# Kernel tuning notes

Measured on AMD Instinct MI355X. Metric: run time of the kernel, lower is better.

Reference implementation:

```python
import jax, jax.numpy as jnp
import numpy as np

B, T, E, H = 2, 2048, 1024, 16
D = E // H  # head dim = 64


def setup_inputs() -> dict:
    key = jax.random.key(0)
    kx, kq, kk, kv, kw = jax.random.split(key, 5)
    # kaiming-normal-like init for per-head projections, xavier-like for output proj
    qkv_std = (2.0 / E) ** 0.5
    w_std = (6.0 / (E + E)) ** 0.5 / (3.0 ** 0.5)
    x = jax.random.normal(kx, (B, T, E), dtype=jnp.float32)
    Wq = jax.random.normal(kq, (H, E, D), dtype=jnp.float32) * qkv_std
    Wk = jax.random.normal(kk, (H, E, D), dtype=jnp.float32) * qkv_std
    Wv = jax.random.normal(kv, (H, E, D), dtype=jnp.float32) * qkv_std
    Wo = jax.random.normal(kw, (E, E), dtype=jnp.float32) * w_std
    return {"x": x, "Wq": Wq, "Wk": Wk, "Wv": Wv, "Wo": Wo}


def reference(x, Wq, Wk, Wv, Wo):
    # per-head projections, batched over heads: bte,hed->bhtd
    q = jnp.einsum('bte,hed->bhtd', x, Wq)
    k = jnp.einsum('bte,hed->bhtd', x, Wk)
    v = jnp.einsum('bte,hed->bhtd', x, Wv)
    scale = 1.0 / jnp.sqrt(jnp.asarray(D, dtype=q.dtype))
    scores = jnp.einsum('bhtd,bhTd->bhtT', q, k) * scale  # [B,H,T,T]
    attn = jax.nn.softmax(scores, axis=-1)
    heads = jnp.einsum('bhtT,bhTd->bhtd', attn, v)  # [B,H,T,D]
    # concat heads along feature dim (head order preserved)
    combined = heads.transpose(0, 2, 1, 3).reshape(B, T, E)
    return combined @ Wo + x
```

## Files before the change

### kernel.cpp

```cpp
#include <hip/hip_runtime.h>
#include <hip/hip_bf16.h>


#define B_ 2
#define T_ 2048
#define E_ 1024
#define H_ 16
#define D_ 64
#define VTS_ 2176
#define LD_ 72

typedef _Float16 h8 __attribute__((ext_vector_type(8)));
typedef float f32x4 __attribute__((ext_vector_type(4)));

union U4 { uint4 u; h8 h; };

__device__ __forceinline__ float h2f(unsigned short s) {
  _Float16 h;
  __builtin_memcpy(&h, &s, 2);
  return (float)h;
}

__device__ __forceinline__ unsigned short f2h(float f) {
  _Float16 h = (_Float16)f;
  unsigned short s;
  __builtin_memcpy(&s, &h, 2);
  return s;
}

template <int CTRL>
__device__ __forceinline__ float dppmv(float x) {
  union { float f; int i; } c;
  c.f = x;
  c.i = __builtin_amdgcn_mov_dpp(c.i, CTRL, 0xF, 0xF, true);
  return c.f;
}

__device__ __forceinline__ float rowmax16(float x) {
  x = fmaxf(x, dppmv<0xB1>(x));
  x = fmaxf(x, dppmv<0x4E>(x));
  x = fmaxf(x, dppmv<0x141>(x));
  x = fmaxf(x, dppmv<0x140>(x));
  return x;
}

__device__ __forceinline__ float rowsum16(float x) {
  x += dppmv<0xB1>(x);
  x += dppmv<0x4E>(x);
  x += dppmv<0x141>(x);
  x += dppmv<0x140>(x);
  return x;
}

__global__ __launch_bounds__(256) void cvt_x(const float* __restrict__ x,
                                             unsigned short* __restrict__ xh) {
  const size_t i = ((size_t)blockIdx.x * 256 + threadIdx.x) * 4;
  const float4 f = *(const float4*)(x + i);
  ushort4 pk;
  pk.x = f2h(f.x); pk.y = f2h(f.y); pk.z = f2h(f.z); pk.w = f2h(f.w);
  *(ushort4*)(xh + i) = pk;
}

__global__ __launch_bounds__(256) void tconv_w(
    const float* __restrict__ Wq, const float* __restrict__ Wk,
    const float* __restrict__ Wv, unsigned short* __restrict__ wt) {
  __shared__ float ts[64][65];
  const int p = blockIdx.z, h = blockIdx.y;
  const float* src = ((p == 0) ? Wq : (p == 1) ? Wk : Wv) + (size_t)h * E_ * D_;
  unsigned short* dst = wt + (size_t)(p * H_ + h) * D_ * E_;
  const int r0 = blockIdx.x * 64;
  const int lr = threadIdx.x >> 4, lc = (threadIdx.x & 15) * 4;
#pragma unroll
  for (int it = 0; it < 4; it++) {
    const float4 f = *(const float4*)(src + (size_t)(r0 + lr + it * 16) * D_ + lc);
    ts[lr + it * 16][lc] = f.x; ts[lr + it * 16][lc + 1] = f.y;
    ts[lr + it * 16][lc + 2] = f.z; ts[lr + it * 16][lc + 3] = f.w;
  }
  __syncthreads();
#pragma unroll
  for (int it = 0; it < 4; it++) {
    const int dr = lr + it * 16;
    ushort4 pk;
    pk.x = f2h(ts[lc + 0][dr]); pk.y = f2h(ts[lc + 1][dr]);
    pk.z = f2h(ts[lc + 2][dr]); pk.w = f2h(ts[lc + 3][dr]);
    *(ushort4*)(dst + (size_t)dr * E_ + r0 + lc) = pk;
  }
}

__global__ __launch_bounds__(256) void tconv_wo(const float* __restrict__ Wo,
                                                unsigned short* __restrict__ wot) {
  __shared__ float ts[64][65];
  const int r0 = blockIdx.x * 64;
  const int c0 = blockIdx.y * 64;
  const int lr = threadIdx.x >> 4, lc = (threadIdx.x & 15) * 4;
#pragma unroll
  for (int it = 0; it < 4; it++) {
    const float4 f = *(const float4*)(Wo + (size_t)(r0 + lr + it * 16) * E_ + c0 + lc);
    ts[lr + it * 16][lc] = f.x; ts[lr + it * 16][lc + 1] = f.y;
    ts[lr + it * 16][lc + 2] = f.z; ts[lr + it * 16][lc + 3] = f.w;
  }
  __syncthreads();
#pragma unroll
  for (int it = 0; it < 4; it++) {
    const int dr = lr + it * 16;
    ushort4 pk;
    pk.x = f2h(ts[lc + 0][dr]); pk.y = f2h(ts[lc + 1][dr]);
    pk.z = f2h(ts[lc + 2][dr]); pk.w = f2h(ts[lc + 3][dr]);
    *(ushort4*)(wot + (size_t)(c0 + dr) * E_ + r0 + lc) = pk;
  }
}

__global__ __launch_bounds__(256) void qkv_mfma(
    const unsigned short* __restrict__ xh, const unsigned short* __restrict__ wt,
    unsigned short* __restrict__ qo, unsigned short* __restrict__ ko,
    unsigned short* __restrict__ vo)
{
  __shared__ unsigned short xs[128 * LD_];
  __shared__ unsigned short wsb[64 * LD_];
  __shared__ unsigned short Cl[4][32 * 72];

  const int tid = threadIdx.x;
  const int w = tid >> 6, lane = tid & 63;
  const int m16 = lane & 15, quad = lane >> 4;
  const int h = blockIdx.y, p = blockIdx.z;
  const int n0 = blockIdx.x * 128;
  const unsigned short* wb = wt + (size_t)(p * H_ + h) * D_ * E_;

  const int sr = tid >> 3;
  const int sc = (tid & 7) * 8;

  f32x4 acc[2][4];
#pragma unroll
  for (int rt = 0; rt < 2; rt++)
#pragma unroll
    for (int ct = 0; ct < 4; ct++) acc[rt][ct] = (f32x4){0.f, 0.f, 0.f, 0.f};

  for (int e0 = 0; e0 < E_; e0 += 64) {
    __syncthreads();
#pragma unroll
    for (int it = 0; it < 4; it++) {
      const int row = it * 32 + sr;
      *(uint4*)(xs + row * LD_ + sc) =
          *(const uint4*)(xh + (size_t)(n0 + row) * E_ + e0 + sc);
    }
#pragma unroll
    for (int it = 0; it < 2; it++) {
      const int row = it * 32 + sr;
      *(uint4*)(wsb + row * LD_ + sc) =
          *(const uint4*)(wb + (size_t)row * E_ + e0 + sc);
    }
    __syncthreads();

#pragma unroll
    for (int kk = 0; kk < 64; kk += 32) {
      U4 a0, a1, bf[4];
      a0.u = *(const uint4*)(xs + (w * 32 + m16) * LD_ + kk + quad * 8);
      a1.u = *(const uint4*)(xs + (w * 32 + 16 + m16) * LD_ + kk + quad * 8);
#pragma unroll
      for (int ct = 0; ct < 4; ct++)
        bf[ct].u = *(const uint4*)(wsb + (ct * 16 + m16) * LD_ + kk + quad * 8);
#pragma unroll
      for (int ct = 0; ct < 4; ct++) {
        acc[0][ct] = __builtin_amdgcn_mfma_f32_16x16x32_f16(a0.h, bf[ct].h, acc[0][ct], 0, 0, 0);
        acc[1][ct] = __builtin_amdgcn_mfma_f32_16x16x32_f16(a1.h, bf[ct].h, acc[1][ct], 0, 0, 0);
      }
    }
  }

  const int nw = n0 + w * 32;
  const int b  = n0 >> 11;
  const int t0 = nw & (T_ - 1);
  const size_t bh = (size_t)(b * H_ + h);

  if (p == 2) {
#pragma unroll
    for (int rt = 0; rt < 2; rt++)
#pragma unroll
      for (int ct = 0; ct < 4; ct++) {
        const int d = ct * 16 + m16;
        const int t = t0 + rt * 16 + quad * 4;
        ushort4 pk;
        pk.x = f2h(acc[rt][ct][0]); pk.y = f2h(acc[rt][ct][1]);
        pk.z = f2h(acc[rt][ct][2]); pk.w = f2h(acc[rt][ct][3]);
        *(ushort4*)(vo + (bh * D_ + d) * (size_t)VTS_ + t) = pk;
      }
  } else {
    unsigned short* outp = (p == 0) ? qo : ko;
    unsigned short* Cw = &Cl[w][0];
#pragma unroll
    for (int rt = 0; rt < 2; rt++)
#pragma unroll
      for (int ct = 0; ct < 4; ct++)
#pragma unroll
        for (int r = 0; r < 4; r++)
          Cw[(rt * 16 + quad * 4 + r) * 72 + ct * 16 + m16] = f2h(acc[rt][ct][r]);
    const int row = lane >> 1;
    const int half = (lane & 1) * 32;
    const uint4 d0 = *(const uint4*)(Cw + row * 72 + half);
    const uint4 d1 = *(const uint4*)(Cw + row * 72 + half + 8);
    const uint4 d2 = *(const uint4*)(Cw + row * 72 + half + 16);
    const uint4 d3 = *(const uint4*)(Cw + row * 72 + half + 24);
    unsigned short* dst = outp + (bh * T_ + t0 + row) * D_ + half;
    *(uint4*)(dst)      = d0;
    *(uint4*)(dst + 8)  = d1;
    *(uint4*)(dst + 16) = d2;
    *(uint4*)(dst + 24) = d3;
  }
}

__global__ __launch_bounds__(256) void attn_kernel(
    const unsigned short* __restrict__ q, const unsigned short* __restrict__ k,
    const unsigned short* __restrict__ vt, unsigned short* __restrict__ comb)
{
  __shared__ unsigned short Kt[64 * LD_];
  __shared__ unsigned short Vt[64 * LD_];
  __shared__ unsigned short Pl[4][16 * LD_];

  const int tid  = threadIdx.x;
  const int w    = tid >> 6;
  const int lane = tid & 63;
  const int m16  = lane & 15;
  const int quad = lane >> 4;
  const int h = blockIdx.y, b = blockIdx.z;
  const size_t bh = (size_t)(b * H_ + h);
  const int q0 = blockIdx.x * 64 + w * 16;

  U4 aQ0, aQ1;
  {
    const unsigned short* qrow = q + (bh * T_ + q0 + m16) * (size_t)D_;
    aQ0.u = *(const uint4*)(qrow + quad * 8);
    aQ1.u = *(const uint4*)(qrow + 32 + quad * 8);
  }

  f32x4 o0 = {0.f, 0.f, 0.f, 0.f}, o1 = o0, o2 = o0, o3 = o0;
  float mrow[4] = {-1e30f, -1e30f, -1e30f, -1e30f};
  float lrow[4] = {0.f, 0.f, 0.f, 0.f};

  const unsigned short* kb  = k  + bh * (size_t)(T_ * D_);
  const unsigned short* vtb = vt + bh * (size_t)(D_ * VTS_);
  unsigned short* Pw = &Pl[w][0];

  const int sr = tid >> 3;
  const int sc = (tid & 7) * 8;

  for (int kt = 0; kt < T_; kt += 64) {
    __syncthreads();
    {
      const uint4 ka = *(const uint4*)(kb + (size_t)(kt + sr) * D_ + sc);
      const uint4 kc = *(const uint4*)(kb + (size_t)(kt + 32 + sr) * D_ + sc);
      *(uint4*)(Kt + sr * LD_ + sc)        = ka;
      *(uint4*)(Kt + (32 + sr) * LD_ + sc) = kc;
      const uint4 va = *(const uint4*)(vtb + (size_t)sr * VTS_ + kt + sc);
      const uint4 vc = *(const uint4*)(vtb + (size_t)(32 + sr) * VTS_ + kt + sc);
      *(uint4*)(Vt + sr * LD_ + sc)        = va;
      *(uint4*)(Vt + (32 + sr) * LD_ + sc) = vc;
    }
    __syncthreads();

    f32x4 s[4];
#pragma unroll
    for (int ct = 0; ct < 4; ct++) {
      U4 kf0, kf1;
      kf0.u = *(const uint4*)(Kt + (ct * 16 + m16) * LD_ + quad * 8);
      kf1.u = *(const uint4*)(Kt + (ct * 16 + m16) * LD_ + 32 + quad * 8);
      f32x4 z = {0.f, 0.f, 0.f, 0.f};
      z = __builtin_amdgcn_mfma_f32_16x16x32_f16(aQ0.h, kf0.h, z, 0, 0, 0);
      z = __builtin_amdgcn_mfma_f32_16x16x32_f16(aQ1.h, kf1.h, z, 0, 0, 0);
      s[ct] = z;
    }

    float al[4];
#pragma unroll
    for (int r = 0; r < 4; r++) {
      const float s0 = s[0][r] * 0.125f;
      const float s1 = s[1][r] * 0.125f;
      const float s2 = s[2][r] * 0.125f;
      const float s3 = s[3][r] * 0.125f;
      const float mt = rowmax16(fmaxf(fmaxf(s0, s1), fmaxf(s2, s3)));
      const float mn = fmaxf(mrow[r], mt);
      const float a  = __expf(mrow[r] - mn);
      const float p0 = __expf(s0 - mn);
      const float p1 = __expf(s1 - mn);
      const float p2 = __expf(s2 - mn);
      const float p3 = __expf(s3 - mn);
      const float rs = rowsum16(p0 + p1 + p2 + p3);
      lrow[r] = lrow[r] * a + rs;
      mrow[r] = mn;
      al[r] = a;
      unsigned short* Pr = Pw + (quad * 4 + r) * LD_ + m16;
      Pr[0]  = f2h(p0);
      Pr[16] = f2h(p1);
      Pr[32] = f2h(p2);
      Pr[48] = f2h(p3);
    }

#pragma unroll
    for (int r = 0; r < 4; r++) {
      o0[r] *= al[r]; o1[r] *= al[r]; o2[r] *= al[r]; o3[r] *= al[r];
    }

    U4 aP0, aP1;
    aP0.u = *(const uint4*)(Pw + m16 * LD_ + quad * 8);
    aP1.u = *(const uint4*)(Pw + m16 * LD_ + 32 + quad * 8);

#pragma unroll
    for (int ct = 0; ct < 4; ct++) {
      U4 vf0, vf1;
      vf0.u = *(const uint4*)(Vt + (ct * 16 + m16) * LD_ + quad * 8);
      vf1.u = *(const uint4*)(Vt + (ct * 16 + m16) * LD_ + 32 + quad * 8);
      f32x4* op = (ct == 0) ? &o0 : (ct == 1) ? &o1 : (ct == 2) ? &o2 : &o3;
      *op = __builtin_amdgcn_mfma_f32_16x16x32_f16(aP0.h, vf0.h, *op, 0, 0, 0);
      *op = __builtin_amdgcn_mfma_f32_16x16x32_f16(aP1.h, vf1.h, *op, 0, 0, 0);
    }
  }

#pragma unroll
  for (int r = 0; r < 4; r++) {
    const float inv = 1.f / lrow[r];
    const int t = q0 + quad * 4 + r;
    unsigned short* dst = comb + ((size_t)b * T_ + t) * E_ + h * D_;
    dst[m16]      = f2h(o0[r] * inv);
    dst[16 + m16] = f2h(o1[r] * inv);
    dst[32 + m16] = f2h(o2[r] * inv);
    dst[48 + m16] = f2h(o3[r] * inv);
  }
}

__global__ __launch_bounds__(256) void out_mfma(
    const unsigned short* __restrict__ comb, const unsigned short* __restrict__ wot,
    const float* __restrict__ x, float* __restrict__ out)
{
  __shared__ unsigned short cs[128 * LD_];
  __shared__ unsigned short wsb[64 * LD_];

  const int tid = threadIdx.x;
  const int w = tid >> 6, lane = tid & 63;
  const int m16 = lane & 15, quad = lane >> 4;
  const int n0 = blockIdx.x * 128;
  const int j0 = blockIdx.y * 64;

  const int sr = tid >> 3;
  const int sc = (tid & 7) * 8;

  f32x4 acc[2][4];
#pragma unroll
  for (int rt = 0; rt < 2; rt++)
#pragma unroll
    for (int ct = 0; ct < 4; ct++) acc[rt][ct] = (f32x4){0.f, 0.f, 0.f, 0.f};

  for (int e0 = 0; e0 < E_; e0 += 64) {
    __syncthreads();
#pragma unroll
    for (int it = 0; it < 4; it++) {
      const int row = it * 32 + sr;
      *(uint4*)(cs + row * LD_ + sc) =
          *(const uint4*)(comb + (size_t)(n0 + row) * E_ + e0 + sc);
    }
#pragma unroll
    for (int it = 0; it < 2; it++) {
      const int row = it * 32 + sr;
      *(uint4*)(wsb + row * LD_ + sc) =
          *(const uint4*)(wot + (size_t)(j0 + row) * E_ + e0 + sc);
    }
    __syncthreads();

#pragma unroll
    for (int kk = 0; kk < 64; kk += 32) {
      U4 a0, a1, bf[4];
      a0.u = *(const uint4*)(cs + (w * 32 + m16) * LD_ + kk + quad * 8);
      a1.u = *(const uint4*)(cs + (w * 32 + 16 + m16) * LD_ + kk + quad * 8);
#pragma unroll
      for (int ct = 0; ct < 4; ct++)
        bf[ct].u = *(const uint4*)(wsb + (ct * 16 + m16) * LD_ + kk + quad * 8);
#pragma unroll
      for (int ct = 0; ct < 4; ct++) {
        acc[0][ct] = __builtin_amdgcn_mfma_f32_16x16x32_f16(a0.h, bf[ct].h, acc[0][ct], 0, 0, 0);
        acc[1][ct] = __builtin_amdgcn_mfma_f32_16x16x32_f16(a1.h, bf[ct].h, acc[1][ct], 0, 0, 0);
      }
    }
  }

  const int nw = n0 + w * 32;
#pragma unroll
  for (int rt = 0; rt < 2; rt++)
#pragma unroll
    for (int r = 0; r < 4; r++) {
      const int n = nw + rt * 16 + quad * 4 + r;
      const float* xr = x + (size_t)n * E_ + j0;
      float* orow = out + (size_t)n * E_ + j0;
#pragma unroll
      for (int ct = 0; ct < 4; ct++) {
        const int j = ct * 16 + m16;
        orow[j] = acc[rt][ct][r] + xr[j];
      }
    }
}

extern "C" void kernel_launch(void* const* d_in, const int* in_sizes, int n_in,
                              void* d_out, int out_size, void* d_ws, size_t ws_size,
                              hipStream_t stream) {
  (void)in_sizes; (void)n_in; (void)out_size; (void)ws_size;

  const float* x  = (const float*)d_in[0];
  const float* Wq = (const float*)d_in[1];
  const float* Wk = (const float*)d_in[2];
  const float* Wv = (const float*)d_in[3];
  const float* Wo = (const float*)d_in[4];
  float* out = (float*)d_out;

  unsigned short* ws0  = (unsigned short*)d_ws;
  unsigned short* xh   = ws0;
  unsigned short* wt   = ws0 + 4194304;
  unsigned short* wot  = ws0 + 7340032;
  unsigned short* qh   = ws0 + 8388608;
  unsigned short* kh   = ws0 + 12582912;
  unsigned short* vth  = ws0 + 16777216;
  unsigned short* comb = xh;

  cvt_x<<<dim3(B_ * T_ * E_ / 1024), dim3(256), 0, stream>>>(x, xh);
  tconv_w<<<dim3(E_ / 64, H_, 3), dim3(256), 0, stream>>>(Wq, Wk, Wv, wt);
  tconv_wo<<<dim3(E_ / 64, E_ / 64), dim3(256), 0, stream>>>(Wo, wot);

  qkv_mfma<<<dim3(B_ * T_ / 128, H_, 3), dim3(256), 0, stream>>>(xh, wt, qh, kh, vth);

  attn_kernel<<<dim3(T_ / 64, H_, B_), dim3(256), 0, stream>>>(qh, kh, vth, comb);

  out_mfma<<<dim3(B_ * T_ / 128, E_ / 64), dim3(256), 0, stream>>>(comb, wot, x, out);
}
```

Before: 239.1 us.

## Double-buffer K/V tiles and keep softmax probabilities in registers for PV MFMA

The attention kernel now double-buffers the K and V tiles in shared memory, prefetching the next tile into registers while the current one is computed. QK^T is computed transposed (K as the A operand), so each lane holds a column of scores. That layout lets P be fed straight from registers into 16x16x16 MFMAs for the PV product, removing the per-wave shared-memory round trip for P. The 1/sqrt(D) scale is folded into Q in fp16, and row reductions use cross-quad shuffles instead of DPP row ops. This trades more shared memory and smaller MFMAs, plus extra shuffles to redistribute alpha and l, for less LDS traffic and fewer stalls from barriers and loads.

Result: faster. 224.4 us (-6.1%).

```diff
diff --git a/kernel.cpp b/kernel.cpp
--- a/kernel.cpp
+++ b/kernel.cpp
@@ -11,6 +11,7 @@
 #define LD_ 72
 
 typedef _Float16 h8 __attribute__((ext_vector_type(8)));
+typedef _Float16 h4 __attribute__((ext_vector_type(4)));
 typedef float f32x4 __attribute__((ext_vector_type(4)));
 
 union U4 { uint4 u; h8 h; };
@@ -26,30 +27,6 @@
   unsigned short s;
   __builtin_memcpy(&s, &h, 2);
   return s;
-}
-
-template <int CTRL>
-__device__ __forceinline__ float dppmv(float x) {
-  union { float f; int i; } c;
-  c.f = x;
-  c.i = __builtin_amdgcn_mov_dpp(c.i, CTRL, 0xF, 0xF, true);
-  return c.f;
-}
-
-__device__ __forceinline__ float rowmax16(float x) {
-  x = fmaxf(x, dppmv<0xB1>(x));
-  x = fmaxf(x, dppmv<0x4E>(x));
-  x = fmaxf(x, dppmv<0x141>(x));
-  x = fmaxf(x, dppmv<0x140>(x));
-  return x;
-}
-
-__device__ __forceinline__ float rowsum16(float x) {
-  x += dppmv<0xB1>(x);
-  x += dppmv<0x4E>(x);
-  x += dppmv<0x141>(x);
-  x += dppmv<0x140>(x);
-  return x;
 }
 
 __global__ __launch_bounds__(256) void cvt_x(const float* __restrict__ x,
@@ -212,9 +189,8 @@
     const unsigned short* __restrict__ q, const unsigned short* __restrict__ k,
     const unsigned short* __restrict__ vt, unsigned short* __restrict__ comb)
 {
-  __shared__ unsigned short Kt[64 * LD_];
-  __shared__ unsigned short Vt[64 * LD_];
-  __shared__ unsigned short Pl[4][16 * LD_];
+  __shared__ unsigned short Kt[2][64 * LD_];
+  __shared__ unsigned short Vt[2][64 * LD_];
 
   const int tid  = threadIdx.x;
   const int w    = tid >> 6;
@@ -230,99 +206,127 @@
     const unsigned short* qrow = q + (bh * T_ + q0 + m16) * (size_t)D_;
     aQ0.u = *(const uint4*)(qrow + quad * 8);
     aQ1.u = *(const uint4*)(qrow + 32 + quad * 8);
+    aQ0.h = aQ0.h * (_Float16)0.125f;
+    aQ1.h = aQ1.h * (_Float16)0.125f;
   }
 
   f32x4 o0 = {0.f, 0.f, 0.f, 0.f}, o1 = o0, o2 = o0, o3 = o0;
-  float mrow[4] = {-1e30f, -1e30f, -1e30f, -1e30f};
-  float lrow[4] = {0.f, 0.f, 0.f, 0.f};
+  float mrow = -1e30f;
+  float lrow = 0.f;
 
   const unsigned short* kb  = k  + bh * (size_t)(T_ * D_);
   const unsigned short* vtb = vt + bh * (size_t)(D_ * VTS_);
-  unsigned short* Pw = &Pl[w][0];
 
   const int sr = tid >> 3;
   const int sc = (tid & 7) * 8;
 
-  for (int kt = 0; kt < T_; kt += 64) {
-    __syncthreads();
-    {
-      const uint4 ka = *(const uint4*)(kb + (size_t)(kt + sr) * D_ + sc);
-      const uint4 kc = *(const uint4*)(kb + (size_t)(kt + 32 + sr) * D_ + sc);
-      *(uint4*)(Kt + sr * LD_ + sc)        = ka;
-      *(uint4*)(Kt + (32 + sr) * LD_ + sc) = kc;
-      const uint4 va = *(const uint4*)(vtb + (size_t)sr * VTS_ + kt + sc);
-      const uint4 vc = *(const uint4*)(vtb + (size_t)(32 + sr) * VTS_ + kt + sc);
-      *(uint4*)(Vt + sr * LD_ + sc)        = va;
-      *(uint4*)(Vt + (32 + sr) * LD_ + sc) = vc;
-    }
-    __syncthreads();
-
-    f32x4 s[4];
+  uint4 kr0, kr1, vr0, vr1;
+  kr0 = *(const uint4*)(kb + (size_t)sr * D_ + sc);
+  kr1 = *(const uint4*)(kb + (size_t)(32 + sr) * D_ + sc);
+  vr0 = *(const uint4*)(vtb + (size_t)sr * VTS_ + sc);
+  vr1 = *(const uint4*)(vtb + (size_t)(32 + sr) * VTS_ + sc);
+  *(uint4*)(&Kt[0][0] + sr * LD_ + sc)        = kr0;
+  *(uint4*)(&Kt[0][0] + (32 + sr) * LD_ + sc) = kr1;
+  *(uint4*)(&Vt[0][0] + sr * LD_ + sc)        = vr0;
+  *(uint4*)(&Vt[0][0] + (32 + sr) * LD_ + sc) = vr1;
+  __syncthreads();
+
+  const int NT = T_ / 64;
+  for (int t = 0; t < NT; t++) {
+    const int cur = t & 1;
+    const unsigned short* Kc = &Kt[cur][0];
+    const unsigned short* Vc = &Vt[cur][0];
+    const bool more = (t + 1 < NT);
+    if (more) {
+      const int kt = (t + 1) * 64;
+      kr0 = *(const uint4*)(kb + (size_t)(kt + sr) * D_ + sc);
+      kr1 = *(const uint4*)(kb + (size_t)(kt + 32 + sr) * D_ + sc);
+      vr0 = *(const uint4*)(vtb + (size_t)sr * VTS_ + kt + sc);
+      vr1 = *(const uint4*)(vtb + (size_t)(32 + sr) * VTS_ + kt + sc);
+    }
+
+    f32x4 st[4];
 #pragma unroll
     for (int ct = 0; ct < 4; ct++) {
       U4 kf0, kf1;
-      kf0.u = *(const uint4*)(Kt + (ct * 16 + m16) * LD_ + quad * 8);
-      kf1.u = *(const uint4*)(Kt + (ct * 16 + m16) * LD_ + 32 + quad * 8);
+      kf0.u = *(const uint4*)(Kc + (ct * 16 + m16) * LD_ + quad * 8);
+      kf1.u = *(const uint4*)(Kc + (ct * 16 + m16) * LD_ + 32 + quad * 8);
       f32x4 z = {0.f, 0.f, 0.f, 0.f};
-      z = __builtin_amdgcn_mfma_f32_16x16x32_f16(aQ0.h, kf0.h, z, 0, 0, 0);
-      z = __builtin_amdgcn_mfma_f32_16x16x32_f16(aQ1.h, kf1.h, z, 0, 0, 0);
-      s[ct] = z;
-    }
+      z = __builtin_amdgcn_mfma_f32_16x16x32_f16(kf0.h, aQ0.h, z, 0, 0, 0);
+      z = __builtin_amdgcn_mfma_f32_16x16x32_f16(kf1.h, aQ1.h, z, 0, 0, 0);
+      st[ct] = z;
+    }
+
+    const float m0 = fmaxf(fmaxf(st[0][0], st[0][1]), fmaxf(st[0][2], st[0][3]));
+    const float m1 = fmaxf(fmaxf(st[1][0], st[1][1]), fmaxf(st[1][2], st[1][3]));
+    const float m2 = fmaxf(fmaxf(st[2][0], st[2][1]), fmaxf(st[2][2], st[2][3]));
+    const float m3 = fmaxf(fmaxf(st[3][0], st[3][1]), fmaxf(st[3][2], st[3][3]));
+    float ml = fmaxf(fmaxf(m0, m1), fmaxf(m2, m3));
+    ml = fmaxf(ml, __shfl_xor(ml, 16));
+    ml = fmaxf(ml, __shfl_xor(ml, 32));
+
+    const float mn = fmaxf(mrow, ml);
+    const float a  = __expf(mrow - mn);
+    mrow = mn;
+
+    float sl = 0.f;
+    h4 pf[4];
+#pragma unroll
+    for (int ct = 0; ct < 4; ct++) {
+      const float e0 = __expf(st[ct][0] - mn);
+      const float e1 = __expf(st[ct][1] - mn);
+      const float e2 = __expf(st[ct][2] - mn);
+      const float e3 = __expf(st[ct][3] - mn);
+      sl += (e0 + e1) + (e2 + e3);
+      pf[ct] = (h4){(_Float16)e0, (_Float16)e1, (_Float16)e2, (_Float16)e3};
+    }
+    sl += __shfl_xor(sl, 16);
+    sl += __shfl_xor(sl, 32);
+    lrow = lrow * a + sl;
 
     float al[4];
 #pragma unroll
-    for (int r = 0; r < 4; r++) {
-      const float s0 = s[0][r] * 0.125f;
-      const float s1 = s[1][r] * 0.125f;
-      const float s2 = s[2][r] * 0.125f;
-      const float s3 = s[3][r] * 0.125f;
-      const float mt = rowmax16(fmaxf(fmaxf(s0, s1), fmaxf(s2, s3)));
-      const float mn = fmaxf(mrow[r], mt);
-      const float a  = __expf(mrow[r] - mn);
-      const float p0 = __expf(s0 - mn);
-      const float p1 = __expf(s1 - mn);
-      const float p2 = __expf(s2 - mn);
-      const float p3 = __expf(s3 - mn);
-      const float rs = rowsum16(p0 + p1 + p2 + p3);
-      lrow[r] = lrow[r] * a + rs;
-      mrow[r] = mn;
-      al[r] = a;
-      unsigned short* Pr = Pw + (quad * 4 + r) * LD_ + m16;
-      Pr[0]  = f2h(p0);
-      Pr[16] = f2h(p1);
-      Pr[32] = f2h(p2);
-      Pr[48] = f2h(p3);
-    }
-
+    for (int r = 0; r < 4; r++) al[r] = __shfl(a, quad * 4 + r);
 #pragma unroll
     for (int r = 0; r < 4; r++) {
       o0[r] *= al[r]; o1[r] *= al[r]; o2[r] *= al[r]; o3[r] *= al[r];
     }
 
-    U4 aP0, aP1;
-    aP0.u = *(const uint4*)(Pw + m16 * LD_ + quad * 8);
-    aP1.u = *(const uint4*)(Pw + m16 * LD_ + 32 + quad * 8);
-
-#pragma unroll
-    for (int ct = 0; ct < 4; ct++) {
-      U4 vf0, vf1;
-      vf0.u = *(const uint4*)(Vt + (ct * 16 + m16) * LD_ + quad * 8);
-      vf1.u = *(const uint4*)(Vt + (ct * 16 + m16) * LD_ + 32 + quad * 8);
-      f32x4* op = (ct == 0) ? &o0 : (ct == 1) ? &o1 : (ct == 2) ? &o2 : &o3;
-      *op = __builtin_amdgcn_mfma_f32_16x16x32_f16(aP0.h, vf0.h, *op, 0, 0, 0);
-      *op = __builtin_amdgcn_mfma_f32_16x16x32_f16(aP1.h, vf1.h, *op, 0, 0, 0);
-    }
-  }
+#pragma unroll
+    for (int ctd = 0; ctd < 4; ctd++) {
+      f32x4* op = (ctd == 0) ? &o0 : (ctd == 1) ? &o1 : (ctd == 2) ? &o2 : &o3;
+      const unsigned short* vrw = Vc + (ctd * 16 + m16) * LD_ + quad * 4;
+#pragma unroll
+      for (int ctk = 0; ctk < 4; ctk++) {
+        const h4 vf = *(const h4*)(vrw + ctk * 16);
+        *op = __builtin_amdgcn_mfma_f32_16x16x16f16(pf[ctk], vf, *op, 0, 0, 0);
+      }
+    }
+
+    if (more) {
+      __syncthreads();
+      unsigned short* Kn = &Kt[cur ^ 1][0];
+      unsigned short* Vn = &Vt[cur ^ 1][0];
+      *(uint4*)(Kn + sr * LD_ + sc)        = kr0;
+      *(uint4*)(Kn + (32 + sr) * LD_ + sc) = kr1;
+      *(uint4*)(Vn + sr * LD_ + sc)        = vr0;
+      *(uint4*)(Vn + (32 + sr) * LD_ + sc) = vr1;
+      __syncthreads();
+    }
+  }
+
+  float linv[4];
+#pragma unroll
+  for (int r = 0; r < 4; r++) linv[r] = 1.f / __shfl(lrow, quad * 4 + r);
 
 #pragma unroll
   for (int r = 0; r < 4; r++) {
-    const float inv = 1.f / lrow[r];
-    const int t = q0 + quad * 4 + r;
-    unsigned short* dst = comb + ((size_t)b * T_ + t) * E_ + h * D_;
-    dst[m16]      = f2h(o0[r] * inv);
-    dst[16 + m16] = f2h(o1[r] * inv);
-    dst[32 + m16] = f2h(o2[r] * inv);
-    dst[48 + m16] = f2h(o3[r] * inv);
+    const int tq = q0 + quad * 4 + r;
+    unsigned short* dst = comb + ((size_t)b * T_ + tq) * E_ + h * D_;
+    dst[m16]      = f2h(o0[r] * linv[r]);
+    dst[16 + m16] = f2h(o1[r] * linv[r]);
+    dst[32 + m16] = f2h(o2[r] * linv[r]);
+    dst[48 + m16] = f2h(o3[r] * linv[r]);
   }
 }
 
```
